# Performance work log

Measured on AMD Instinct MI355X. Metric: run time of the kernel, lower is better.

## Reference

```python
import jax, jax.numpy as jnp
import numpy as np

B, T, I, H, L, S = 128, 256, 256, 256, 4, 3


def _gru(x_t, w_i, b_i, b_h):
    # torch.nn.GRUCell called WITHOUT hx in the source => hidden state is 0,
    # so Whh @ 0 vanishes and only the b_hh bias contributes to the gates.
    gi = x_t @ w_i.T + b_i                      # [B, 3H]
    hh = b_h.shape[0] // 3
    i_r, i_z, i_n = gi[:, :hh], gi[:, hh:2 * hh], gi[:, 2 * hh:]
    h_r, h_z, h_n = b_h[:hh], b_h[hh:2 * hh], b_h[2 * hh:]
    r = jax.nn.sigmoid(i_r + h_r)
    z = jax.nn.sigmoid(i_z + h_z)
    n = jnp.tanh(i_n + r * h_n)
    return (1.0 - z) * n                        # + z * 0


def setup_inputs() -> dict:
    key = jax.random.key(0)
    ks = jax.random.split(key, 12)
    s = 1.0 / np.sqrt(H)
    u = lambda k, shape: jax.random.uniform(k, shape, jnp.float32, -s, s)
    return {
        "x": jax.random.normal(ks[0], (B, T, I), jnp.float32),
        "hidden": jax.random.normal(ks[1], (B, L, L), jnp.float32),
        "w_ih0": u(ks[2], (S, 3 * H, I)),      # layer-0 input weights, per split
        "b_ih0": u(ks[3], (S, 3 * H)),
        "b_hh0": u(ks[4], (S, 3 * H)),
        "w_ih": u(ks[5], (S, L - 1, 3 * H, H)),  # layers 1..L-1
        "b_ih": u(ks[6], (S, L - 1, 3 * H)),
        "b_hh": u(ks[7], (S, L - 1, 3 * H)),
        "w_lw": u(ks[8], (L, H)),              # layer_weights: Linear(H -> L)
        "b_lw": u(ks[9], (L,)),
        "w_sel": u(ks[10], (S, H + I)),        # selective_layer: Linear(H+I -> S)
        "b_sel": u(ks[11], (S,)),
    }


def reference(x, hidden, w_ih0, b_ih0, b_hh0, w_ih, b_ih, b_hh, w_lw, b_lw, w_sel, b_sel):
    Lm1 = w_ih.shape[1]

    def run_stack(x_t, cur):
        # cur is a (possibly traced) int index selecting one of S GRU stacks
        hs = [_gru(x_t, w_ih0[cur], b_ih0[cur], b_hh0[cur])]
        for l in range(Lm1):
            hs.append(_gru(hs[-1], w_ih[cur, l], b_ih[cur, l], b_hh[cur, l]))
        return jnp.stack(hs, axis=1)            # [B, L, H]

    h0 = run_stack(x[:, 0, :], 0)               # first step always uses stack 0

    def step(h, x_t):
        energy = h @ w_lw.T + b_lw              # [B, L, L]
        attn = jnp.sum(hidden * energy, axis=2) # [B, L]
        a = jax.nn.softmax(attn, axis=1)
        ctx = jnp.einsum('bl,blh->bh', a, h)    # [B, H]
        scores = jnp.concatenate([ctx, x_t], axis=1) @ w_sel.T + b_sel  # [B, S]
        cur = jnp.argmax(jnp.sum(scores, axis=0))  # batch-summed routing
        h_new = run_stack(x_t, cur)
        return h_new, h_new[:, -1, :]

    h_final, ys = jax.lax.scan(step, h0, jnp.swapaxes(x[:, 1:, :], 0, 1))
    outputs = jnp.concatenate([h0[:, -1:, :], jnp.swapaxes(ys, 0, 1)], axis=1)  # [B, T, H]
    return outputs, h_final[:, -1, :]
```

## Files before the change

### kernel.cpp

```cpp
#include <hip/hip_runtime.h>
#include <math.h>

#define Bsz 128
#define Tsz 256
#define Isz 256
#define Hsz 256
#define Lsz 4
#define Ssz 3
#define Mrows (Bsz*Tsz)

using f16x8 = __attribute__((ext_vector_type(8))) _Float16;
using f32x4 = __attribute__((ext_vector_type(4))) float;

#define LOG2E 1.44269504f
#define GEMM_BLOCKS 768

__global__ __launch_bounds__(256) void f32_to_f16_3(
    const float* __restrict__ s0, _Float16* __restrict__ d0, int n0,
    const float* __restrict__ s1, _Float16* __restrict__ d1, int n1,
    const float* __restrict__ s2, _Float16* __restrict__ d2, int n2)
{
  int idx = blockIdx.x * 256 + threadIdx.x;
  const float* s; _Float16* d;
  if (idx < n0)           { s = s0; d = d0; }
  else if (idx < n0 + n1) { idx -= n0; s = s1; d = d1; }
  else                    { idx -= n0 + n1; if (idx >= n2) return; s = s2; d = d2; }
  const float4 v0 = *(const float4*)(s + (size_t)idx * 8);
  const float4 v1 = *(const float4*)(s + (size_t)idx * 8 + 4);
  _Float16 h[8];
  h[0] = (_Float16)v0.x; h[1] = (_Float16)v0.y;
  h[2] = (_Float16)v0.z; h[3] = (_Float16)v0.w;
  h[4] = (_Float16)v1.x; h[5] = (_Float16)v1.y;
  h[6] = (_Float16)v1.z; h[7] = (_Float16)v1.w;
  *(uint4*)(d + (size_t)idx * 8) = *(uint4*)h;
}

__global__ __launch_bounds__(256, 2) void gemm_gru_f16(
    const _Float16* __restrict__ Abase, size_t a_cur_stride,
    const _Float16* __restrict__ Wbase, size_t w_cur_stride,
    const float* __restrict__ bi_g, size_t bi_stride,
    const float* __restrict__ bh_g, size_t bh_stride,
    _Float16* __restrict__ Hout,
    const float* __restrict__ w_lw, const float* __restrict__ w_sel,
    float* __restrict__ e_out, float* __restrict__ p_out, int layer_ep)
{
  __shared__ __align__(16) char smem[49152];
  const int tid = threadIdx.x;
  const int bid = blockIdx.x;

  if (bid >= GEMM_BLOCKS) {
    float (*wc)[256]   = (float(*)[256])smem;
    float (*ps)[64][8] = (float(*)[64][8])(smem + 7 * 256 * 4);
    const size_t mg0 = (size_t)(bid - GEMM_BLOCKS) * 64;

    #pragma unroll
    for (int j = 0; j < 7; j++)
      wc[j][tid] = (j < 4) ? w_lw[j * 256 + tid] : w_sel[(j - 4) * 512 + tid];
    __syncthreads();

    const int r = tid & 63, pp = tid >> 6;
    const _Float16* hrow = Abase + (mg0 + r) * 256 + pp * 64;
    float acc[7] = {0.f, 0.f, 0.f, 0.f, 0.f, 0.f, 0.f};
    #pragma unroll
    for (int i = 0; i < 8; i++) {
      union { uint4 u; _Float16 h[8]; } hv;
      hv.u = *(const uint4*)(hrow + i * 8);
      float hf[8];
      #pragma unroll
      for (int k = 0; k < 8; k++) hf[k] = (float)hv.h[k];
      #pragma unroll
      for (int j = 0; j < 7; j++) {
        const float4 w0 = *(const float4*)&wc[j][pp * 64 + i * 8];
        const float4 w1 = *(const float4*)&wc[j][pp * 64 + i * 8 + 4];
        acc[j] += hf[0] * w0.x + hf[1] * w0.y + hf[2] * w0.z + hf[3] * w0.w
                + hf[4] * w1.x + hf[5] * w1.y + hf[6] * w1.z + hf[7] * w1.w;
      }
    }
    #pragma unroll
    for (int j = 0; j < 7; j++) ps[pp][r][j] = acc[j];
    __syncthreads();

    if (tid < 64) {
      float d[7];
      #pragma unroll
      for (int j = 0; j < 7; j++)
        d[j] = ps[0][tid][j] + ps[1][tid][j] + ps[2][tid][j] + ps[3][tid][j];
      const size_t mg = mg0 + tid;
      const int cc = (int)(mg >> 15);
      const int m  = (int)(mg & 32767);
      const int b = m >> 8, t = m & 255;
      const size_t base = ((size_t)cc * Tsz + t) * Bsz + b;
      #pragma unroll
      for (int j = 0; j < 4; j++) e_out[base * 16 + layer_ep * 4 + j] = d[j];
      #pragma unroll
      for (int j = 0; j < 3; j++) p_out[base * 12 + layer_ep * 3 + j] = d[4 + j];
    }
    return;
  }

  const int cu   = bid >> 8;
  const int n0   = ((bid >> 6) & 3) * 64;
  const int rmb  = (bid & 63) * 512;

  _Float16 (*AhS)[8192] = (_Float16(*)[8192])smem;

  const _Float16* A = Abase + (size_t)cu * a_cur_stride;
  const _Float16* W = Wbase + (size_t)cu * w_cur_stride;
  const float* bi = bi_g + (size_t)cu * bi_stride;
  const float* bh = bh_g + (size_t)cu * bh_stride;

  const int lane = tid & 63;
  const int wv   = tid >> 6;
  const int q    = lane >> 4;
  const int c    = lane & 15;

  const int ncol = n0 + wv * 16 + c;
  f16x8 wf[3][8];
  #pragma unroll
  for (int s = 0; s < 3; s++)
    #pragma unroll
    for (int k0 = 0; k0 < 8; k0++)
      wf[s][k0] = *(const f16x8*)(W + (size_t)(s * 256 + ncol) * 256 + k0 * 32 + q * 8);
  #pragma unroll
  for (int s = 0; s < 3; s++)
    #pragma unroll
    for (int k0 = 0; k0 < 8; k0++)
      asm volatile("" : "+v"(wf[s][k0]));

  const float c0  = -LOG2E * (bi[ncol] + bh[ncol]);
  const float c1  =  LOG2E * (bi[256 + ncol] + bh[256 + ncol]);
  const float c3  = 2.f * LOG2E * bi[512 + ncol];
  const float bhn = bh[512 + ncol];

  f32x4 acc[3][2];

  auto stage = [&](int buf, int ch) {
    const int rm = rmb + ch * 32;
    #pragma unroll
    for (int i = 0; i < 4; i++) {
      const int p0 = 8 * wv + 2 * i;
      const int pk = p0 + (lane >> 5);
      const _Float16* src = A + (size_t)(rm + (lane & 31)) * 256 + pk * 8;
      __builtin_amdgcn_global_load_lds(
          (const __attribute__((address_space(1))) void*)src,
          (__attribute__((address_space(3))) void*)&AhS[buf][p0 * 256],
          16, 0, 0);
    }
  };

  auto compute_chunk = [&](int buf, int ch) {
    const int rm = rmb + ch * 32;
    #pragma unroll
    for (int s = 0; s < 3; s++)
      #pragma unroll
      for (int mi = 0; mi < 2; mi++)
        acc[s][mi] = (f32x4)0.f;
    #pragma unroll
    for (int k0 = 0; k0 < 8; k0++) {
      const f16x8 a0 = *(const f16x8*)&AhS[buf][(k0 * 4 + q) * 256 + c * 8];
      const f16x8 a1 = *(const f16x8*)&AhS[buf][(k0 * 4 + q) * 256 + 128 + c * 8];
      #pragma unroll
      for (int s = 0; s < 3; s++) {
        acc[s][0] = __builtin_amdgcn_mfma_f32_16x16x32_f16(a0, wf[s][k0], acc[s][0], 0, 0, 0);
        acc[s][1] = __builtin_amdgcn_mfma_f32_16x16x32_f16(a1, wf[s][k0], acc[s][1], 0, 0, 0);
      }
    }
    #pragma unroll
    for (int mi = 0; mi < 2; mi++) {
      #pragma unroll
      for (int reg = 0; reg < 4; reg++) {
        const float ar = acc[0][mi][reg];
        const float az = acc[1][mi][reg];
        const float an = acc[2][mi][reg];
        const float e0 = __builtin_amdgcn_exp2f(fmaf(-LOG2E, ar, c0));
        const float r  = __builtin_amdgcn_rcpf(1.f + e0);
        const float e1 = __builtin_amdgcn_exp2f(fmaf(LOG2E, az, c1));
        const float tt = fmaf(r, bhn, an);
        const float a2 = fminf(fmaf(2.f * LOG2E, tt, c3), 120.f);
        const float e2 = __builtin_amdgcn_exp2f(a2);
        const float out = (e2 - 1.f) *
            __builtin_amdgcn_rcpf((1.f + e1) * (1.f + e2));
        const size_t row = (size_t)cu * Mrows + rm + mi * 16 + q * 4 + reg;
        Hout[row * 256 + ncol] = (_Float16)out;
      }
    }
  };

  stage(0, 0);
  stage(1, 1);
  asm volatile("s_waitcnt vmcnt(4)" ::: "memory");
  __builtin_amdgcn_s_barrier();

  int bc = 0;
  for (int t = 0; t < 14; ++t) {
    int bs = bc + 2; if (bs >= 3) bs -= 3;
    stage(bs, t + 2);
    compute_chunk(bc, t);
    asm volatile("s_waitcnt vmcnt(12)" ::: "memory");
    __builtin_amdgcn_s_barrier();
    bc = (bc + 1 == 3) ? 0 : bc + 1;
  }
  compute_chunk(bc, 14);
  asm volatile("s_waitcnt vmcnt(0)" ::: "memory");
  __builtin_amdgcn_s_barrier();
  bc = (bc + 1 == 3) ? 0 : bc + 1;
  compute_chunk(bc, 15);
}

__global__ __launch_bounds__(256) void ep_tile(
    const _Float16* __restrict__ Hh,
    const float* __restrict__ w_lw, const float* __restrict__ w_sel, int layer,
    float* __restrict__ e, float* __restrict__ p)
{
  __shared__ float wc[7][256];
  __shared__ float ps[4][64][8];
  const int tid = threadIdx.x;
  const size_t mg0 = (size_t)blockIdx.x * 64;

  #pragma unroll
  for (int j = 0; j < 7; j++)
    wc[j][tid] = (j < 4) ? w_lw[j * 256 + tid] : w_sel[(j - 4) * 512 + tid];
  __syncthreads();

  const int r = tid & 63, pp = tid >> 6;
  const _Float16* hrow = Hh + (mg0 + r) * 256 + pp * 64;
  float acc[7] = {0.f, 0.f, 0.f, 0.f, 0.f, 0.f, 0.f};
  #pragma unroll
  for (int i = 0; i < 8; i++) {
    union { uint4 u; _Float16 h[8]; } hv;
    hv.u = *(const uint4*)(hrow + i * 8);
    float hf[8];
    #pragma unroll
    for (int k = 0; k < 8; k++) hf[k] = (float)hv.h[k];
    #pragma unroll
    for (int j = 0; j < 7; j++) {
      const float4 w0 = *(const float4*)&wc[j][pp * 64 + i * 8];
      const float4 w1 = *(const float4*)&wc[j][pp * 64 + i * 8 + 4];
      acc[j] += hf[0] * w0.x + hf[1] * w0.y + hf[2] * w0.z + hf[3] * w0.w
              + hf[4] * w1.x + hf[5] * w1.y + hf[6] * w1.z + hf[7] * w1.w;
    }
  }
  #pragma unroll
  for (int j = 0; j < 7; j++) ps[pp][r][j] = acc[j];
  __syncthreads();

  if (tid < 64) {
    float d[7];
    #pragma unroll
    for (int j = 0; j < 7; j++)
      d[j] = ps[0][tid][j] + ps[1][tid][j] + ps[2][tid][j] + ps[3][tid][j];
    const size_t mg = mg0 + tid;
    const int cc = (int)(mg >> 15);
    const int m  = (int)(mg & 32767);
    const int b = m >> 8, t = m & 255;
    const size_t base = ((size_t)cc * Tsz + t) * Bsz + b;
    #pragma unroll
    for (int j = 0; j < 4; j++) e[base * 16 + layer * 4 + j] = d[j];
    #pragma unroll
    for (int j = 0; j < 3; j++) p[base * 12 + layer * 3 + j] = d[4 + j];
  }
}

__global__ __launch_bounds__(128) void attn_xs(
    const float* __restrict__ e, const float* __restrict__ p,
    const float* __restrict__ hidden, const float* __restrict__ b_lw,
    const float* __restrict__ x, const float* __restrict__ w_sel,
    const float* __restrict__ b_sel,
    float* __restrict__ score_h, float* __restrict__ xs)
{
  __shared__ float red[2][3];
  const int t = blockIdx.x;
  const int wv = threadIdx.x >> 6, ln = threadIdx.x & 63;

  if (blockIdx.y < 3) {
    const int cc = blockIdx.y;
    const int b = threadIdx.x;
    const float* eb = e + ((size_t)(cc * Tsz + t) * Bsz + b) * 16;
    const float* pb = p + ((size_t)(cc * Tsz + t) * Bsz + b) * 12;
    const float* hb = hidden + b * 16;
    const float bl0 = b_lw[0], bl1 = b_lw[1], bl2 = b_lw[2], bl3 = b_lw[3];
    float attn[4];
    #pragma unroll
    for (int i = 0; i < 4; i++) {
      attn[i] = hb[i * 4 + 0] * (eb[i * 4 + 0] + bl0)
              + hb[i * 4 + 1] * (eb[i * 4 + 1] + bl1)
              + hb[i * 4 + 2] * (eb[i * 4 + 2] + bl2)
              + hb[i * 4 + 3] * (eb[i * 4 + 3] + bl3);
    }
    const float mx = fmaxf(fmaxf(attn[0], attn[1]), fmaxf(attn[2], attn[3]));
    float ex[4], sum = 0.f;
    #pragma unroll
    for (int i = 0; i < 4; i++) { ex[i] = expf(attn[i] - mx); sum += ex[i]; }
    const float inv = 1.f / sum;
    float sc[3];
    #pragma unroll
    for (int s = 0; s < 3; s++) {
      float v = 0.f;
      #pragma unroll
      for (int i = 0; i < 4; i++) v += ex[i] * pb[i * 3 + s];
      sc[s] = v * inv;
    }
    #pragma unroll
    for (int off = 32; off; off >>= 1)
      #pragma unroll
      for (int s = 0; s < 3; s++) sc[s] += __shfl_xor(sc[s], off);
    if (ln == 0) { red[wv][0] = sc[0]; red[wv][1] = sc[1]; red[wv][2] = sc[2]; }
    __syncthreads();
    if (threadIdx.x == 0) {
      #pragma unroll
      for (int s = 0; s < 3; s++)
        score_h[((size_t)cc * Tsz + t) * 3 + s] = red[0][s] + red[1][s];
    }
  } else {
    const int k = threadIdx.x;
    float s0 = 0.f, s1 = 0.f;
    for (int b = 0; b < Bsz; b++) {
      const float* xb = x + ((size_t)b * Tsz + t) * Isz;
      s0 += xb[k]; s1 += xb[k + 128];
    }
    float pr[3];
    #pragma unroll
    for (int qq = 0; qq < 3; qq++)
      pr[qq] = s0 * w_sel[qq * (Hsz + Isz) + Hsz + k]
             + s1 * w_sel[qq * (Hsz + Isz) + Hsz + k + 128];
    #pragma unroll
    for (int off = 32; off; off >>= 1)
      #pragma unroll
      for (int qq = 0; qq < 3; qq++) pr[qq] += __shfl_xor(pr[qq], off);
    if (ln == 0) { red[wv][0] = pr[0]; red[wv][1] = pr[1]; red[wv][2] = pr[2]; }
    __syncthreads();
    if (threadIdx.x == 0) {
      #pragma unroll
      for (int qq = 0; qq < 3; qq++)
        xs[t * 3 + qq] = red[0][qq] + red[1][qq] + (float)Bsz * b_sel[qq];
    }
  }
}

__global__ __launch_bounds__(256) void select_kernel(
    const float* __restrict__ score_h, const float* __restrict__ xs,
    int* __restrict__ cur)
{
  __shared__ unsigned S[Tsz];
  const int t = threadIdx.x;

  unsigned m = 0x24;
  if (t >= 1) {
    m = 0;
    const float* xr = xs + t * 3;
    #pragma unroll
    for (int cc = 0; cc < 3; cc++) {
      const float* sh = score_h + ((size_t)cc * Tsz + (t - 1)) * 3;
      const float v0 = sh[0] + xr[0];
      const float v1 = sh[1] + xr[1];
      const float v2 = sh[2] + xr[2];
      unsigned best = 0; float bv = v0;
      if (v1 > bv) { bv = v1; best = 1; }
      if (v2 > bv) { bv = v2; best = 2; }
      m |= best << (2 * cc);
    }
  }
  S[t] = m;
  __syncthreads();

  #pragma unroll
  for (int d = 1; d < Tsz; d <<= 1) {
    const unsigned prev = (t >= d) ? S[t - d] : 0x24u;
    const unsigned self = S[t];
    __syncthreads();
    unsigned comp = 0;
    #pragma unroll
    for (int xx = 0; xx < 3; xx++) {
      const unsigned y = (prev >> (2 * xx)) & 3u;
      const unsigned z = (self >> (2 * y)) & 3u;
      comp |= z << (2 * xx);
    }
    S[t] = comp;
    __syncthreads();
  }
  cur[t] = (int)(S[t] & 3u);
}

__global__ __launch_bounds__(256) void gather_out(
    const _Float16* __restrict__ Hh, const int* __restrict__ cur,
    float* __restrict__ out)
{
  const size_t idx = ((size_t)blockIdx.x * 256 + threadIdx.x) * 4;
  const size_t BTH = (size_t)Bsz * Tsz * Hsz;
  int b, t, h;
  if (idx < BTH) {
    b = (int)(idx >> 16);
    const int rem = (int)(idx & 65535);
    t = rem >> 8; h = rem & 255;
  } else {
    const size_t r2 = idx - BTH;
    b = (int)(r2 >> 8); h = (int)(r2 & 255); t = Tsz - 1;
  }
  const int cc = cur[t];
  const size_t g = (((size_t)cc * Mrows + (size_t)b * Tsz + t) * Hsz + h);
  union { ushort4 u; _Float16 hv[4]; } cv;
  cv.u = *(const ushort4*)(Hh + g);
  float4 v;
  v.x = (float)cv.hv[0]; v.y = (float)cv.hv[1];
  v.z = (float)cv.hv[2]; v.w = (float)cv.hv[3];
  *(float4*)(out + idx) = v;
}

extern "C" void kernel_launch(void* const* d_in, const int* in_sizes, int n_in,
                              void* d_out, int out_size, void* d_ws, size_t ws_size,
                              hipStream_t stream) {
  const float* x      = (const float*)d_in[0];
  const float* hidden = (const float*)d_in[1];
  const float* w_ih0  = (const float*)d_in[2];
  const float* b_ih0  = (const float*)d_in[3];
  const float* b_hh0  = (const float*)d_in[4];
  const float* w_ih   = (const float*)d_in[5];
  const float* b_ih   = (const float*)d_in[6];
  const float* b_hh   = (const float*)d_in[7];
  const float* w_lw   = (const float*)d_in[8];
  const float* b_lw   = (const float*)d_in[9];
  const float* w_sel  = (const float*)d_in[10];
  const float* b_sel  = (const float*)d_in[11];
  float* out = (float*)d_out;

  char* w = (char*)d_ws;
  const size_t HN = (size_t)3 * Mrows * 256;
  const size_t XN = (size_t)Bsz * Tsz * Isz;
  const size_t W0N = (size_t)3 * 768 * 256;
  const size_t WLN = (size_t)3 * 3 * 768 * 256;
  _Float16* HA  = (_Float16*)w; w += HN * 2;
  _Float16* HB  = (_Float16*)w; w += HN * 2;
  _Float16* xh  = (_Float16*)w; w += XN * 2;
  _Float16* Wh0 = (_Float16*)w; w += W0N * 2;
  _Float16* WhL = (_Float16*)w; w += WLN * 2;
  float* e       = (float*)w; w += (size_t)3 * Tsz * Bsz * 16 * 4;
  float* p       = (float*)w; w += (size_t)3 * Tsz * Bsz * 12 * 4;
  float* score_h = (float*)w; w += (size_t)3 * Tsz * 3 * 4;
  float* xsb     = (float*)w; w += (size_t)Tsz * 3 * 4;
  int*   curb    = (int*)w;   w += (size_t)Tsz * 4;

  f32_to_f16_3<<<5248, 256, 0, stream>>>(
      x, xh, (int)(XN / 8),
      w_ih0, Wh0, (int)(W0N / 8),
      w_ih, WhL, (int)(WLN / 8));

  gemm_gru_f16<<<GEMM_BLOCKS, 256, 0, stream>>>(
      xh, (size_t)0, Wh0, (size_t)768 * 256,
      b_ih0, (size_t)768, b_hh0, (size_t)768, HA,
      nullptr, nullptr, nullptr, nullptr, -1);

  const size_t wcur = (size_t)3 * 768 * 256;
  const size_t bst  = (size_t)3 * 768;
  _Float16* ping = HA; _Float16* pong = HB;
  for (int l = 1; l < 4; l++) {
    gemm_gru_f16<<<GEMM_BLOCKS + 1536, 256, 0, stream>>>(
        ping, (size_t)Mrows * 256,
        WhL + (size_t)(l - 1) * 768 * 256, wcur,
        b_ih + (size_t)(l - 1) * 768, bst,
        b_hh + (size_t)(l - 1) * 768, bst, pong,
        w_lw, w_sel, e, p, l - 1);
    _Float16* t1 = ping; ping = pong; pong = t1;
  }
  ep_tile<<<(3 * Mrows) / 64, 256, 0, stream>>>(ping, w_lw, w_sel, 3, e, p);

  attn_xs<<<dim3(Tsz, 4), 128, 0, stream>>>(
      e, p, hidden, b_lw, x, w_sel, b_sel, score_h, xsb);
  select_kernel<<<1, 256, 0, stream>>>(score_h, xsb, curb);
  gather_out<<<8224, 256, 0, stream>>>(ping, curb, out);
}
```

Measured before the change: 365.5 us.

## Fuse last-layer epilogue into attention kernel and scan into gather

Folds the layer-3 projection (ep_tile) into the attention/score kernel, so the e/p values for the last layer are computed in registers and never round-trip through global memory. It also merges the single-block selection scan with the output gather: each of 2048 blocks recomputes the 256-step prefix composition redundantly and then grid-strides over the output. Two kernel launches and their global intermediates go away. In exchange every gather block repeats the scan, and the fused attention kernel now runs 256 threads per block with extra shared memory.

```diff
diff --git a/kernel.cpp b/kernel.cpp
--- a/kernel.cpp
+++ b/kernel.cpp
@@ -207,129 +207,126 @@
   compute_chunk(bc, 15);
 }
 
-__global__ __launch_bounds__(256) void ep_tile(
+__global__ __launch_bounds__(256) void attn_ep_xs(
     const _Float16* __restrict__ Hh,
-    const float* __restrict__ w_lw, const float* __restrict__ w_sel, int layer,
-    float* __restrict__ e, float* __restrict__ p)
-{
-  __shared__ float wc[7][256];
-  __shared__ float ps[4][64][8];
-  const int tid = threadIdx.x;
-  const size_t mg0 = (size_t)blockIdx.x * 64;
-
-  #pragma unroll
-  for (int j = 0; j < 7; j++)
-    wc[j][tid] = (j < 4) ? w_lw[j * 256 + tid] : w_sel[(j - 4) * 512 + tid];
-  __syncthreads();
-
-  const int r = tid & 63, pp = tid >> 6;
-  const _Float16* hrow = Hh + (mg0 + r) * 256 + pp * 64;
-  float acc[7] = {0.f, 0.f, 0.f, 0.f, 0.f, 0.f, 0.f};
-  #pragma unroll
-  for (int i = 0; i < 8; i++) {
-    union { uint4 u; _Float16 h[8]; } hv;
-    hv.u = *(const uint4*)(hrow + i * 8);
-    float hf[8];
-    #pragma unroll
-    for (int k = 0; k < 8; k++) hf[k] = (float)hv.h[k];
-    #pragma unroll
-    for (int j = 0; j < 7; j++) {
-      const float4 w0 = *(const float4*)&wc[j][pp * 64 + i * 8];
-      const float4 w1 = *(const float4*)&wc[j][pp * 64 + i * 8 + 4];
-      acc[j] += hf[0] * w0.x + hf[1] * w0.y + hf[2] * w0.z + hf[3] * w0.w
-              + hf[4] * w1.x + hf[5] * w1.y + hf[6] * w1.z + hf[7] * w1.w;
-    }
-  }
-  #pragma unroll
-  for (int j = 0; j < 7; j++) ps[pp][r][j] = acc[j];
-  __syncthreads();
-
-  if (tid < 64) {
-    float d[7];
-    #pragma unroll
-    for (int j = 0; j < 7; j++)
-      d[j] = ps[0][tid][j] + ps[1][tid][j] + ps[2][tid][j] + ps[3][tid][j];
-    const size_t mg = mg0 + tid;
-    const int cc = (int)(mg >> 15);
-    const int m  = (int)(mg & 32767);
-    const int b = m >> 8, t = m & 255;
-    const size_t base = ((size_t)cc * Tsz + t) * Bsz + b;
-    #pragma unroll
-    for (int j = 0; j < 4; j++) e[base * 16 + layer * 4 + j] = d[j];
-    #pragma unroll
-    for (int j = 0; j < 3; j++) p[base * 12 + layer * 3 + j] = d[4 + j];
-  }
-}
-
-__global__ __launch_bounds__(128) void attn_xs(
     const float* __restrict__ e, const float* __restrict__ p,
     const float* __restrict__ hidden, const float* __restrict__ b_lw,
     const float* __restrict__ x, const float* __restrict__ w_sel,
-    const float* __restrict__ b_sel,
+    const float* __restrict__ b_sel, const float* __restrict__ w_lw,
     float* __restrict__ score_h, float* __restrict__ xs)
 {
+  __shared__ float wc[7][256];
+  __shared__ float ps[128][2][7];
   __shared__ float red[2][3];
+  const int tid = threadIdx.x;
   const int t = blockIdx.x;
-  const int wv = threadIdx.x >> 6, ln = threadIdx.x & 63;
+  const int lane = tid & 63, wid = tid >> 6;
 
   if (blockIdx.y < 3) {
     const int cc = blockIdx.y;
-    const int b = threadIdx.x;
-    const float* eb = e + ((size_t)(cc * Tsz + t) * Bsz + b) * 16;
-    const float* pb = p + ((size_t)(cc * Tsz + t) * Bsz + b) * 12;
-    const float* hb = hidden + b * 16;
-    const float bl0 = b_lw[0], bl1 = b_lw[1], bl2 = b_lw[2], bl3 = b_lw[3];
-    float attn[4];
-    #pragma unroll
-    for (int i = 0; i < 4; i++) {
-      attn[i] = hb[i * 4 + 0] * (eb[i * 4 + 0] + bl0)
-              + hb[i * 4 + 1] * (eb[i * 4 + 1] + bl1)
-              + hb[i * 4 + 2] * (eb[i * 4 + 2] + bl2)
-              + hb[i * 4 + 3] * (eb[i * 4 + 3] + bl3);
-    }
-    const float mx = fmaxf(fmaxf(attn[0], attn[1]), fmaxf(attn[2], attn[3]));
-    float ex[4], sum = 0.f;
-    #pragma unroll
-    for (int i = 0; i < 4; i++) { ex[i] = expf(attn[i] - mx); sum += ex[i]; }
-    const float inv = 1.f / sum;
-    float sc[3];
-    #pragma unroll
-    for (int s = 0; s < 3; s++) {
-      float v = 0.f;
-      #pragma unroll
-      for (int i = 0; i < 4; i++) v += ex[i] * pb[i * 3 + s];
-      sc[s] = v * inv;
-    }
-    #pragma unroll
-    for (int off = 32; off; off >>= 1)
-      #pragma unroll
-      for (int s = 0; s < 3; s++) sc[s] += __shfl_xor(sc[s], off);
-    if (ln == 0) { red[wv][0] = sc[0]; red[wv][1] = sc[1]; red[wv][2] = sc[2]; }
-    __syncthreads();
-    if (threadIdx.x == 0) {
+    #pragma unroll
+    for (int j = 0; j < 7; j++)
+      wc[j][tid] = (j < 4) ? w_lw[j * 256 + tid] : w_sel[(j - 4) * 512 + tid];
+    __syncthreads();
+
+    const int b  = tid & 127;
+    const int hi = tid >> 7;
+    const _Float16* hrow =
+        Hh + ((size_t)cc * Mrows + (size_t)b * Tsz + t) * 256;
+
+    float qa[7] = {0.f,0.f,0.f,0.f,0.f,0.f,0.f};
+    float qb[7] = {0.f,0.f,0.f,0.f,0.f,0.f,0.f};
+    auto quarter = [&](float (&qacc)[7], int pp) {
+      #pragma unroll
+      for (int i = 0; i < 8; i++) {
+        union { uint4 u; _Float16 hh[8]; } hv;
+        hv.u = *(const uint4*)(hrow + pp * 64 + i * 8);
+        float hf[8];
+        #pragma unroll
+        for (int k = 0; k < 8; k++) hf[k] = (float)hv.hh[k];
+        #pragma unroll
+        for (int j = 0; j < 7; j++) {
+          const float4 w0 = *(const float4*)&wc[j][pp * 64 + i * 8];
+          const float4 w1 = *(const float4*)&wc[j][pp * 64 + i * 8 + 4];
+          qacc[j] += hf[0]*w0.x + hf[1]*w0.y + hf[2]*w0.z + hf[3]*w0.w
+                   + hf[4]*w1.x + hf[5]*w1.y + hf[6]*w1.z + hf[7]*w1.w;
+        }
+      }
+    };
+    quarter(qa, hi * 2);
+    quarter(qb, hi * 2 + 1);
+
+    if (hi) {
+      #pragma unroll
+      for (int j = 0; j < 7; j++) { ps[b][0][j] = qa[j]; ps[b][1][j] = qb[j]; }
+    }
+    __syncthreads();
+    if (!hi) {
+      float d[7];
+      #pragma unroll
+      for (int j = 0; j < 7; j++)
+        d[j] = ((qa[j] + qb[j]) + ps[b][0][j]) + ps[b][1][j];
+
+      const size_t base = ((size_t)cc * Tsz + t) * Bsz + b;
+      const float* eb = e + base * 16;
+      const float* pb = p + base * 12;
+      const float* hb = hidden + b * 16;
+      const float bl0 = b_lw[0], bl1 = b_lw[1], bl2 = b_lw[2], bl3 = b_lw[3];
+      float attn[4];
+      #pragma unroll
+      for (int i = 0; i < 3; i++) {
+        attn[i] = hb[i*4+0]*(eb[i*4+0]+bl0) + hb[i*4+1]*(eb[i*4+1]+bl1)
+                + hb[i*4+2]*(eb[i*4+2]+bl2) + hb[i*4+3]*(eb[i*4+3]+bl3);
+      }
+      attn[3] = hb[12]*(d[0]+bl0) + hb[13]*(d[1]+bl1)
+              + hb[14]*(d[2]+bl2) + hb[15]*(d[3]+bl3);
+      const float mx = fmaxf(fmaxf(attn[0],attn[1]), fmaxf(attn[2],attn[3]));
+      float ex[4], sum = 0.f;
+      #pragma unroll
+      for (int i = 0; i < 4; i++) { ex[i] = expf(attn[i]-mx); sum += ex[i]; }
+      const float inv = 1.f / sum;
+      float sc[3];
+      #pragma unroll
+      for (int s = 0; s < 3; s++) {
+        float v = 0.f;
+        #pragma unroll
+        for (int i = 0; i < 3; i++) v += ex[i] * pb[i*3+s];
+        v += ex[3] * d[4+s];
+        sc[s] = v * inv;
+      }
+      #pragma unroll
+      for (int off = 32; off; off >>= 1)
+        #pragma unroll
+        for (int s = 0; s < 3; s++) sc[s] += __shfl_xor(sc[s], off);
+      if (lane == 0) { red[wid][0]=sc[0]; red[wid][1]=sc[1]; red[wid][2]=sc[2]; }
+    }
+    __syncthreads();
+    if (tid == 0) {
       #pragma unroll
       for (int s = 0; s < 3; s++)
         score_h[((size_t)cc * Tsz + t) * 3 + s] = red[0][s] + red[1][s];
     }
   } else {
-    const int k = threadIdx.x;
-    float s0 = 0.f, s1 = 0.f;
-    for (int b = 0; b < Bsz; b++) {
-      const float* xb = x + ((size_t)b * Tsz + t) * Isz;
-      s0 += xb[k]; s1 += xb[k + 128];
-    }
-    float pr[3];
-    #pragma unroll
-    for (int qq = 0; qq < 3; qq++)
-      pr[qq] = s0 * w_sel[qq * (Hsz + Isz) + Hsz + k]
-             + s1 * w_sel[qq * (Hsz + Isz) + Hsz + k + 128];
-    #pragma unroll
-    for (int off = 32; off; off >>= 1)
-      #pragma unroll
-      for (int qq = 0; qq < 3; qq++) pr[qq] += __shfl_xor(pr[qq], off);
-    if (ln == 0) { red[wv][0] = pr[0]; red[wv][1] = pr[1]; red[wv][2] = pr[2]; }
-    __syncthreads();
-    if (threadIdx.x == 0) {
+    if (tid < 128) {
+      const int k = tid;
+      float s0 = 0.f, s1 = 0.f;
+      for (int b2 = 0; b2 < Bsz; b2++) {
+        const float* xb = x + ((size_t)b2 * Tsz + t) * Isz;
+        s0 += xb[k]; s1 += xb[k + 128];
+      }
+      float pr[3];
+      #pragma unroll
+      for (int qq = 0; qq < 3; qq++)
+        pr[qq] = s0 * w_sel[qq * (Hsz + Isz) + Hsz + k]
+               + s1 * w_sel[qq * (Hsz + Isz) + Hsz + k + 128];
+      #pragma unroll
+      for (int off = 32; off; off >>= 1)
+        #pragma unroll
+        for (int qq = 0; qq < 3; qq++) pr[qq] += __shfl_xor(pr[qq], off);
+      if (lane == 0) { red[wid][0]=pr[0]; red[wid][1]=pr[1]; red[wid][2]=pr[2]; }
+    }
+    __syncthreads();
+    if (tid == 0) {
       #pragma unroll
       for (int qq = 0; qq < 3; qq++)
         xs[t * 3 + qq] = red[0][qq] + red[1][qq] + (float)Bsz * b_sel[qq];
@@ -337,20 +334,21 @@
   }
 }
 
-__global__ __launch_bounds__(256) void select_kernel(
+__global__ __launch_bounds__(256) void scan_gather(
+    const _Float16* __restrict__ Hh,
     const float* __restrict__ score_h, const float* __restrict__ xs,
-    int* __restrict__ cur)
+    float* __restrict__ out)
 {
   __shared__ unsigned S[Tsz];
-  const int t = threadIdx.x;
+  const int tid = threadIdx.x;
 
   unsigned m = 0x24;
-  if (t >= 1) {
+  if (tid >= 1) {
     m = 0;
-    const float* xr = xs + t * 3;
+    const float* xr = xs + tid * 3;
     #pragma unroll
     for (int cc = 0; cc < 3; cc++) {
-      const float* sh = score_h + ((size_t)cc * Tsz + (t - 1)) * 3;
+      const float* sh = score_h + ((size_t)cc * Tsz + (tid - 1)) * 3;
       const float v0 = sh[0] + xr[0];
       const float v1 = sh[1] + xr[1];
       const float v2 = sh[2] + xr[2];
@@ -360,13 +358,13 @@
       m |= best << (2 * cc);
     }
   }
-  S[t] = m;
+  S[tid] = m;
   __syncthreads();
 
   #pragma unroll
-  for (int d = 1; d < Tsz; d <<= 1) {
-    const unsigned prev = (t >= d) ? S[t - d] : 0x24u;
-    const unsigned self = S[t];
+  for (int dd = 1; dd < Tsz; dd <<= 1) {
+    const unsigned prev = (tid >= dd) ? S[tid - dd] : 0x24u;
+    const unsigned self = S[tid];
     __syncthreads();
     unsigned comp = 0;
     #pragma unroll
@@ -375,35 +373,33 @@
       const unsigned z = (self >> (2 * y)) & 3u;
       comp |= z << (2 * xx);
     }
-    S[t] = comp;
-    __syncthreads();
-  }
-  cur[t] = (int)(S[t] & 3u);
-}
-
-__global__ __launch_bounds__(256) void gather_out(
-    const _Float16* __restrict__ Hh, const int* __restrict__ cur,
-    float* __restrict__ out)
-{
-  const size_t idx = ((size_t)blockIdx.x * 256 + threadIdx.x) * 4;
+    S[tid] = comp;
+    __syncthreads();
+  }
+
   const size_t BTH = (size_t)Bsz * Tsz * Hsz;
-  int b, t, h;
-  if (idx < BTH) {
-    b = (int)(idx >> 16);
-    const int rem = (int)(idx & 65535);
-    t = rem >> 8; h = rem & 255;
-  } else {
-    const size_t r2 = idx - BTH;
-    b = (int)(r2 >> 8); h = (int)(r2 & 255); t = Tsz - 1;
-  }
-  const int cc = cur[t];
-  const size_t g = (((size_t)cc * Mrows + (size_t)b * Tsz + t) * Hsz + h);
-  union { ushort4 u; _Float16 hv[4]; } cv;
-  cv.u = *(const ushort4*)(Hh + g);
-  float4 v;
-  v.x = (float)cv.hv[0]; v.y = (float)cv.hv[1];
-  v.z = (float)cv.hv[2]; v.w = (float)cv.hv[3];
-  *(float4*)(out + idx) = v;
+  const size_t N4 = (BTH + (size_t)Bsz * Hsz) / 4;
+  for (size_t i4 = (size_t)blockIdx.x * 256 + tid; i4 < N4;
+       i4 += (size_t)gridDim.x * 256) {
+    const size_t idx = i4 * 4;
+    int b, t, h;
+    if (idx < BTH) {
+      b = (int)(idx >> 16);
+      const int rem = (int)(idx & 65535);
+      t = rem >> 8; h = rem & 255;
+    } else {
+      const size_t r2 = idx - BTH;
+      b = (int)(r2 >> 8); h = (int)(r2 & 255); t = Tsz - 1;
+    }
+    const int cc = (int)(S[t] & 3u);
+    const size_t g = (((size_t)cc * Mrows + (size_t)b * Tsz + t) * Hsz + h);
+    union { ushort4 u; _Float16 hv[4]; } cv;
+    cv.u = *(const ushort4*)(Hh + g);
+    float4 v;
+    v.x = (float)cv.hv[0]; v.y = (float)cv.hv[1];
+    v.z = (float)cv.hv[2]; v.w = (float)cv.hv[3];
+    *(float4*)(out + idx) = v;
+  }
 }
 
 extern "C" void kernel_launch(void* const* d_in, const int* in_sizes, int n_in,
@@ -437,7 +433,6 @@
   float* p       = (float*)w; w += (size_t)3 * Tsz * Bsz * 12 * 4;
   float* score_h = (float*)w; w += (size_t)3 * Tsz * 3 * 4;
   float* xsb     = (float*)w; w += (size_t)Tsz * 3 * 4;
-  int*   curb    = (int*)w;   w += (size_t)Tsz * 4;
 
   f32_to_f16_3<<<5248, 256, 0, stream>>>(
       x, xh, (int)(XN / 8),
@@ -461,10 +456,9 @@
         w_lw, w_sel, e, p, l - 1);
     _Float16* t1 = ping; ping = pong; pong = t1;
   }
-  ep_tile<<<(3 * Mrows) / 64, 256, 0, stream>>>(ping, w_lw, w_sel, 3, e, p);
-
-  attn_xs<<<dim3(Tsz, 4), 128, 0, stream>>>(
-      e, p, hidden, b_lw, x, w_sel, b_sel, score_h, xsb);
-  select_kernel<<<1, 256, 0, stream>>>(score_h, xsb, curb);
-  gather_out<<<8224, 256, 0, stream>>>(ping, curb, out);
+
+  attn_ep_xs<<<dim3(Tsz, 4), 256, 0, stream>>>(
+      ping, e, p, hidden, b_lw, x, w_sel, b_sel, w_lw, score_h, xsb);
+
+  scan_gather<<<2048, 256, 0, stream>>>(ping, score_h, xsb, out);
 }
```

New measurement: 359.4 us. Within noise of the previous version (-1.7%).
